# Optimization experiments

Hardware: AMD Instinct MI355X
Metric: run time of the kernel (lower is better)

The kernel has to match this reference:

```python
import jax, jax.numpy as jnp
import numpy as np


def setup_inputs() -> dict:
    key = jax.random.key(0)
    k1, k2 = jax.random.split(key)
    B, P, H, W, D, C = 4, 8, 32, 32, 32, 16
    input_fmap = jax.random.normal(k1, (B, P, H, W, D, C), dtype=jnp.float32)
    # theta ~ identity affine (rows act on [y, x, z, 1]) + small noise so most
    # sampled coordinates fall inside the volume
    base = jnp.concatenate([jnp.eye(3, dtype=jnp.float32), jnp.zeros((3, 1), jnp.float32)], axis=1)
    theta = base[None, None] + 0.1 * jax.random.normal(k2, (B, P, 3, 4), dtype=jnp.float32)
    return {"input_fmap": input_fmap, "theta": theta}


def reference(input_fmap, theta):
    B, P, H, W, D, C = input_fmap.shape
    # --- affine grid generation (matches tf.meshgrid 'xy' indexing) ---
    xs = jnp.arange(W, dtype=jnp.float32)
    ys = jnp.arange(H, dtype=jnp.float32)
    zs = jnp.arange(D, dtype=jnp.float32)
    x_t, y_t, z_t = jnp.meshgrid(xs, ys, zs, indexing="xy")  # each (H, W, D)
    grid = jnp.stack([y_t.ravel(), x_t.ravel(), z_t.ravel(),
                      jnp.ones(H * W * D, jnp.float32)], axis=0)  # (4, HWD)
    batch_grids = jnp.einsum("bpij,jn->bpin", theta, grid)  # (B, P, 3, HWD)
    batch_grids = batch_grids.reshape(B, P, 3, H, W, D)
    y_s = batch_grids[:, :, 0]
    x_s = batch_grids[:, :, 1]
    z_s = batch_grids[:, :, 2]

    # --- trilinear sampling on a 2-voxel zero-padded volume ---
    fmap_p = jnp.pad(input_fmap, ((0, 0), (0, 0), (2, 2), (2, 2), (2, 2), (0, 0)))
    x = x_s + 2.0
    y = y_s + 2.0
    z = z_s + 2.0
    # NOTE: original code clips all three axes with H + 2 (faithful reproduction)
    hi = H + 2
    x0 = jnp.clip(jnp.floor(x).astype(jnp.int32), 0, hi)
    y0 = jnp.clip(jnp.floor(y).astype(jnp.int32), 0, hi)
    z0 = jnp.clip(jnp.floor(z).astype(jnp.int32), 0, hi)
    x1, y1, z1 = x0 + 1, y0 + 1, z0 + 1

    b_idx = jnp.arange(B)[:, None, None, None, None]
    p_idx = jnp.arange(P)[None, :, None, None, None]

    def gather(yy, xx, zz):
        # indices stacked as [y, x, z] in the original -> axes (H_pad, W_pad, D_pad)
        return fmap_p[b_idx, p_idx, yy, xx, zz]  # (B, P, H, W, D, C)

    c000 = gather(y0, x0, z0)
    c001 = gather(y0, x0, z1)
    c010 = gather(y1, x0, z0)
    c011 = gather(y1, x0, z1)
    c100 = gather(y0, x1, z0)
    c101 = gather(y0, x1, z1)
    c110 = gather(y1, x1, z0)
    c111 = gather(y1, x1, z1)

    xd = (x - x0.astype(jnp.float32))[..., None]
    yd = (y - y0.astype(jnp.float32))[..., None]
    zd = (z - z0.astype(jnp.float32))[..., None]

    out = (c000 * (1 - xd) * (1 - yd) * (1 - zd)
           + c100 * xd * (1 - yd) * (1 - zd)
           + c010 * (1 - xd) * yd * (1 - zd)
           + c001 * (1 - xd) * (1 - yd) * zd
           + c101 * xd * (1 - yd) * zd
           + c011 * (1 - xd) * yd * zd
           + c110 * xd * yd * (1 - zd)
           + c111 * xd * yd * zd)
    return out
```

## Files before the change

### kernel.cpp

```cpp
#include <hip/hip_runtime.h>

constexpr int B = 4, P = 8, H = 32, W = 32, D = 32, C = 16;

constexpr int TI = 4, TJ = 4, TK = 8;
constexpr int VOLCAP = 960;

using f32x4 = __attribute__((ext_vector_type(4))) float;
using f16x8 = __attribute__((ext_vector_type(8))) _Float16;

__global__ __launch_bounds__(256) void resample_tile(
    const float* __restrict__ fmap,
    const float* __restrict__ theta,
    float* __restrict__ out)
{
    __shared__ _Float16 sm[VOLCAP * 16];

    const int orig = blockIdx.x;
    const int virt = (orig & 7) * 1024 + (orig >> 3);
    const int bp = virt >> 8;
    const int t6 = virt & 255;
    const int i0 = (t6 >> 5) * TI;
    const int j0 = ((t6 >> 2) & 7) * TJ;
    const int k0 = (t6 & 3) * TK;

    const float4* th4 = (const float4*)(theta + bp * 12);
    const float4 t0 = th4[0];
    const float4 t1 = th4[1];
    const float4 t2 = th4[2];

    const float fi0 = (float)i0, fj0 = (float)j0, fk0 = (float)k0;
    const float pyb = fmaf(t0.x, fi0, fmaf(t0.y, fj0, fmaf(t0.z, fk0, t0.w))) + 2.f;
    const float pxb = fmaf(t1.x, fi0, fmaf(t1.y, fj0, fmaf(t1.z, fk0, t1.w))) + 2.f;
    const float pzb = fmaf(t2.x, fi0, fmaf(t2.y, fj0, fmaf(t2.z, fk0, t2.w))) + 2.f;

    const float eyi = t0.x * (TI - 1), eyj = t0.y * (TJ - 1), eyk = t0.z * (TK - 1);
    const float exi = t1.x * (TI - 1), exj = t1.y * (TJ - 1), exk = t1.z * (TK - 1);
    const float ezi = t2.x * (TI - 1), ezj = t2.y * (TJ - 1), ezk = t2.z * (TK - 1);

    const float pymin = pyb + fminf(eyi, 0.f) + fminf(eyj, 0.f) + fminf(eyk, 0.f);
    const float pymax = pyb + fmaxf(eyi, 0.f) + fmaxf(eyj, 0.f) + fmaxf(eyk, 0.f);
    const float pxmin = pxb + fminf(exi, 0.f) + fminf(exj, 0.f) + fminf(exk, 0.f);
    const float pxmax = pxb + fmaxf(exi, 0.f) + fmaxf(exj, 0.f) + fmaxf(exk, 0.f);
    const float pzmin = pzb + fminf(ezi, 0.f) + fminf(ezj, 0.f) + fminf(ezk, 0.f);
    const float pzmax = pzb + fmaxf(ezi, 0.f) + fmaxf(ezj, 0.f) + fmaxf(ezk, 0.f);

    const int tylo = max(0, min((int)fminf(fmaxf(floorf(pymin), 0.f), 34.f) - 2, 31));
    int       tyhi = min(31, (int)fminf(fmaxf(floorf(pymax), 0.f), 34.f) - 1);
    tyhi = max(tyhi, tylo);
    const int txlo = max(0, min((int)fminf(fmaxf(floorf(pxmin), 0.f), 34.f) - 2, 31));
    int       txhi = min(31, (int)fminf(fmaxf(floorf(pxmax), 0.f), 34.f) - 1);
    txhi = max(txhi, txlo);
    const int tzlo = max(0, min((int)fminf(fmaxf(floorf(pzmin), 0.f), 34.f) - 2, 31));
    int       tzhi = min(31, (int)fminf(fmaxf(floorf(pzmax), 0.f), 34.f) - 1);
    tzhi = max(tzhi, tzlo);

    const int dy = tyhi - tylo + 1;
    const int dx = txhi - txlo + 1;
    const int dz = tzhi - tzlo + 1;
    const int vol = dy * dx * dz;
    const bool fast = (vol <= VOLCAP) && (dy <= 20) && (dx <= 20) && (dz <= 20);

    const float* slice = fmap + bp * (H * W * D * C);

    if (fast) {
        const unsigned mdz = 0xFFFFu / (unsigned)dz + 1u;
        const unsigned mdx = 0xFFFFu / (unsigned)dx + 1u;
        const int nch = vol * 2;
        for (int s = threadIdx.x; s < nch; s += 256) {
            const int vf = s >> 1, hh = s & 1;
            const int row = (int)(((unsigned)vf * mdz) >> 16);
            const int zl  = vf - row * dz;
            const int ry  = (int)(((unsigned)row * mdx) >> 16);
            const int rx  = row - ry * dx;
            const float* g = slice
                + (((tylo + ry) * W + (txlo + rx)) * D + (tzlo + zl)) * C + hh * 8;
            const f32x4 a = *(const f32x4*)g;
            const f32x4 b = *(const f32x4*)(g + 4);
            f16x8 hv;
            hv[0] = (_Float16)a[0]; hv[1] = (_Float16)a[1];
            hv[2] = (_Float16)a[2]; hv[3] = (_Float16)a[3];
            hv[4] = (_Float16)b[0]; hv[5] = (_Float16)b[1];
            hv[6] = (_Float16)b[2]; hv[7] = (_Float16)b[3];
            *(f16x8*)(sm + vf * 16 + hh * 8) = hv;
        }
    }
    __syncthreads();

    const int h8 = threadIdx.x & 1;
    const int v  = threadIdx.x >> 1;
    const int lk = v & 7;
    const int lj = (v >> 3) & 3;
    const int li = v >> 5;

    const float fi = (float)(i0 + li), fj = (float)(j0 + lj), fk = (float)(k0 + lk);
    const float py = fmaf(t0.x, fi, fmaf(t0.y, fj, fmaf(t0.z, fk, t0.w))) + 2.f;
    const float px = fmaf(t1.x, fi, fmaf(t1.y, fj, fmaf(t1.z, fk, t1.w))) + 2.f;
    const float pz = fmaf(t2.x, fi, fmaf(t2.y, fj, fmaf(t2.z, fk, t2.w))) + 2.f;

    const float fy0 = fminf(fmaxf(floorf(py), 0.f), 34.f);
    const float fx0 = fminf(fmaxf(floorf(px), 0.f), 34.f);
    const float fz0 = fminf(fmaxf(floorf(pz), 0.f), 34.f);
    const float yd = py - fy0, xd = px - fx0, zd = pz - fz0;
    const int ty0 = (int)fy0 - 2, tx0 = (int)fx0 - 2, tz0 = (int)fz0 - 2;

    float wy[2], wx[2], wz[2];
    int   iy[2], ix[2], iz[2];
    wy[0] = ((unsigned)ty0       < (unsigned)H) ? (1.0f - yd) : 0.0f;
    wy[1] = ((unsigned)(ty0 + 1) < (unsigned)H) ? yd          : 0.0f;
    wx[0] = ((unsigned)tx0       < (unsigned)W) ? (1.0f - xd) : 0.0f;
    wx[1] = ((unsigned)(tx0 + 1) < (unsigned)W) ? xd          : 0.0f;
    wz[0] = ((unsigned)tz0       < (unsigned)D) ? (1.0f - zd) : 0.0f;
    wz[1] = ((unsigned)(tz0 + 1) < (unsigned)D) ? zd          : 0.0f;
    iy[0] = min(max(ty0, 0), H - 1);  iy[1] = min(max(ty0 + 1, 0), H - 1);
    ix[0] = min(max(tx0, 0), W - 1);  ix[1] = min(max(tx0 + 1, 0), W - 1);
    iz[0] = min(max(tz0, 0), D - 1);  iz[1] = min(max(tz0 + 1, 0), D - 1);

    f32x4 r0, r1;

    if (fast) {
        int ly[2], lx[2], lz[2];
        ly[0] = min(max(iy[0] - tylo, 0), dy - 1);
        ly[1] = min(max(iy[1] - tylo, 0), dy - 1);
        lx[0] = min(max(ix[0] - txlo, 0), dx - 1);
        lx[1] = min(max(ix[1] - txlo, 0), dx - 1);
        lz[0] = min(max(iz[0] - tzlo, 0), dz - 1);
        lz[1] = min(max(iz[1] - tzlo, 0), dz - 1);

        f16x8 aA = 0, aB = 0;
        #pragma unroll
        for (int a = 0; a < 2; ++a)
            #pragma unroll
            for (int b2 = 0; b2 < 2; ++b2)
                #pragma unroll
                for (int c2 = 0; c2 < 2; ++c2) {
                    const int cn = a * 4 + b2 * 2 + c2;
                    const int vf = (ly[a] * dx + lx[b2]) * dz + lz[c2];
                    const f16x8 d = *(const f16x8*)(sm + vf * 16 + h8 * 8);
                    const _Float16 hw = (_Float16)(wy[a] * wx[b2] * wz[c2]);
                    const f16x8 hv = {hw, hw, hw, hw, hw, hw, hw, hw};
                    if (cn < 4) aA += hv * d; else aB += hv * d;
                }
        r0[0] = (float)aA[0] + (float)aB[0];
        r0[1] = (float)aA[1] + (float)aB[1];
        r0[2] = (float)aA[2] + (float)aB[2];
        r0[3] = (float)aA[3] + (float)aB[3];
        r1[0] = (float)aA[4] + (float)aB[4];
        r1[1] = (float)aA[5] + (float)aB[5];
        r1[2] = (float)aA[6] + (float)aB[6];
        r1[3] = (float)aA[7] + (float)aB[7];
    } else {
        const float* gb = slice + h8 * 8;
        f32x4 acc0 = {0,0,0,0}, acc1 = {0,0,0,0};
        #pragma unroll
        for (int a = 0; a < 2; ++a)
            #pragma unroll
            for (int b2 = 0; b2 < 2; ++b2)
                #pragma unroll
                for (int c2 = 0; c2 < 2; ++c2) {
                    const float wgt = wy[a] * wx[b2] * wz[c2];
                    const float* p = gb + ((iy[a] * W + ix[b2]) * D + iz[c2]) * C;
                    acc0 += wgt * *(const f32x4*)p;
                    acc1 += wgt * *(const f32x4*)(p + 4);
                }
        r0 = acc0; r1 = acc1;
    }

    float* op = out + (((bp * H + (i0 + li)) * W + (j0 + lj)) * D + (k0 + lk)) * C
                    + h8 * 8;
    *(f32x4*)op       = r0;
    *(f32x4*)(op + 4) = r1;
}

extern "C" void kernel_launch(void* const* d_in, const int* in_sizes, int n_in,
                              void* d_out, int out_size, void* d_ws, size_t ws_size,
                              hipStream_t stream) {
    const float* fmap  = (const float*)d_in[0];
    const float* theta = (const float*)d_in[1];
    float* out = (float*)d_out;

    const int grid = (B * P * H * W * D) / (TI * TJ * TK);
    resample_tile<<<grid, 256, 0, stream>>>(fmap, theta, out);
}
```

Measured before the change: 28.86 us.

## Double output tile per block and assign one voxel's 16 channels per thread

Doubles the output tile along j (4x8x8 voxels per block), so the neighbourhood staged in shared memory covers more outputs and the grid holds half as many blocks. Each thread now handles all 16 channels of one voxel instead of 8, with full 64-byte loads and stores in both the staging and the compute phase. This is meant to cut redundant halo loads and per-voxel index arithmetic, at the cost of a larger shared-memory buffer, more registers per thread and fewer blocks in flight. The fast path also switches to summing the fp16 partial accumulators in fp16 before converting to fp32.

```diff
diff --git a/kernel.cpp b/kernel.cpp
--- a/kernel.cpp
+++ b/kernel.cpp
@@ -2,8 +2,8 @@
 
 constexpr int B = 4, P = 8, H = 32, W = 32, D = 32, C = 16;
 
-constexpr int TI = 4, TJ = 4, TK = 8;
-constexpr int VOLCAP = 960;
+constexpr int TI = 4, TJ = 8, TK = 8;
+constexpr int VOLCAP = 1152;
 
 using f32x4 = __attribute__((ext_vector_type(4))) float;
 using f16x8 = __attribute__((ext_vector_type(8))) _Float16;
@@ -16,12 +16,12 @@
     __shared__ _Float16 sm[VOLCAP * 16];
 
     const int orig = blockIdx.x;
-    const int virt = (orig & 7) * 1024 + (orig >> 3);
-    const int bp = virt >> 8;
-    const int t6 = virt & 255;
-    const int i0 = (t6 >> 5) * TI;
-    const int j0 = ((t6 >> 2) & 7) * TJ;
-    const int k0 = (t6 & 3) * TK;
+    const int virt = (orig & 7) * 512 + (orig >> 3);
+    const int bp = virt >> 7;
+    const int t7 = virt & 127;
+    const int i0 = (t7 >> 4) * TI;
+    const int j0 = ((t7 >> 2) & 3) * TJ;
+    const int k0 = (t7 & 3) * TK;
 
     const float4* th4 = (const float4*)(theta + bp * 12);
     const float4 t0 = th4[0];
@@ -65,32 +65,36 @@
     if (fast) {
         const unsigned mdz = 0xFFFFu / (unsigned)dz + 1u;
         const unsigned mdx = 0xFFFFu / (unsigned)dx + 1u;
-        const int nch = vol * 2;
-        for (int s = threadIdx.x; s < nch; s += 256) {
-            const int vf = s >> 1, hh = s & 1;
-            const int row = (int)(((unsigned)vf * mdz) >> 16);
-            const int zl  = vf - row * dz;
+        for (int s = threadIdx.x; s < vol; s += 256) {
+            const int row = (int)(((unsigned)s * mdz) >> 16);
+            const int zl  = s - row * dz;
             const int ry  = (int)(((unsigned)row * mdx) >> 16);
             const int rx  = row - ry * dx;
             const float* g = slice
-                + (((tylo + ry) * W + (txlo + rx)) * D + (tzlo + zl)) * C + hh * 8;
-            const f32x4 a = *(const f32x4*)g;
-            const f32x4 b = *(const f32x4*)(g + 4);
-            f16x8 hv;
-            hv[0] = (_Float16)a[0]; hv[1] = (_Float16)a[1];
-            hv[2] = (_Float16)a[2]; hv[3] = (_Float16)a[3];
-            hv[4] = (_Float16)b[0]; hv[5] = (_Float16)b[1];
-            hv[6] = (_Float16)b[2]; hv[7] = (_Float16)b[3];
-            *(f16x8*)(sm + vf * 16 + hh * 8) = hv;
+                + (((tylo + ry) * W + (txlo + rx)) * D + (tzlo + zl)) * C;
+            const f32x4 a  = *(const f32x4*)g;
+            const f32x4 b2 = *(const f32x4*)(g + 4);
+            const f32x4 c  = *(const f32x4*)(g + 8);
+            const f32x4 d4 = *(const f32x4*)(g + 12);
+            f16x8 lo, hi;
+            lo[0] = (_Float16)a[0];  lo[1] = (_Float16)a[1];
+            lo[2] = (_Float16)a[2];  lo[3] = (_Float16)a[3];
+            lo[4] = (_Float16)b2[0]; lo[5] = (_Float16)b2[1];
+            lo[6] = (_Float16)b2[2]; lo[7] = (_Float16)b2[3];
+            hi[0] = (_Float16)c[0];  hi[1] = (_Float16)c[1];
+            hi[2] = (_Float16)c[2];  hi[3] = (_Float16)c[3];
+            hi[4] = (_Float16)d4[0]; hi[5] = (_Float16)d4[1];
+            hi[6] = (_Float16)d4[2]; hi[7] = (_Float16)d4[3];
+            *(f16x8*)(sm + s * 16)     = lo;
+            *(f16x8*)(sm + s * 16 + 8) = hi;
         }
     }
     __syncthreads();
 
-    const int h8 = threadIdx.x & 1;
-    const int v  = threadIdx.x >> 1;
-    const int lk = v & 7;
-    const int lj = (v >> 3) & 3;
-    const int li = v >> 5;
+    const int tid = threadIdx.x;
+    const int lk = tid & 7;
+    const int lj = (tid >> 3) & 7;
+    const int li = tid >> 6;
 
     const float fi = (float)(i0 + li), fj = (float)(j0 + lj), fk = (float)(k0 + lk);
     const float py = fmaf(t0.x, fi, fmaf(t0.y, fj, fmaf(t0.z, fk, t0.w))) + 2.f;
@@ -104,53 +108,59 @@
     const int ty0 = (int)fy0 - 2, tx0 = (int)fx0 - 2, tz0 = (int)fz0 - 2;
 
     float wy[2], wx[2], wz[2];
-    int   iy[2], ix[2], iz[2];
     wy[0] = ((unsigned)ty0       < (unsigned)H) ? (1.0f - yd) : 0.0f;
     wy[1] = ((unsigned)(ty0 + 1) < (unsigned)H) ? yd          : 0.0f;
     wx[0] = ((unsigned)tx0       < (unsigned)W) ? (1.0f - xd) : 0.0f;
     wx[1] = ((unsigned)(tx0 + 1) < (unsigned)W) ? xd          : 0.0f;
     wz[0] = ((unsigned)tz0       < (unsigned)D) ? (1.0f - zd) : 0.0f;
     wz[1] = ((unsigned)(tz0 + 1) < (unsigned)D) ? zd          : 0.0f;
-    iy[0] = min(max(ty0, 0), H - 1);  iy[1] = min(max(ty0 + 1, 0), H - 1);
-    ix[0] = min(max(tx0, 0), W - 1);  ix[1] = min(max(tx0 + 1, 0), W - 1);
-    iz[0] = min(max(tz0, 0), D - 1);  iz[1] = min(max(tz0 + 1, 0), D - 1);
 
-    f32x4 r0, r1;
+    f32x4 r0, r1, r2, r3;
 
     if (fast) {
         int ly[2], lx[2], lz[2];
-        ly[0] = min(max(iy[0] - tylo, 0), dy - 1);
-        ly[1] = min(max(iy[1] - tylo, 0), dy - 1);
-        lx[0] = min(max(ix[0] - txlo, 0), dx - 1);
-        lx[1] = min(max(ix[1] - txlo, 0), dx - 1);
-        lz[0] = min(max(iz[0] - tzlo, 0), dz - 1);
-        lz[1] = min(max(iz[1] - tzlo, 0), dz - 1);
+        ly[0] = min(max(ty0     - tylo, 0), dy - 1);
+        ly[1] = min(max(ty0 + 1 - tylo, 0), dy - 1);
+        lx[0] = min(max(tx0     - txlo, 0), dx - 1);
+        lx[1] = min(max(tx0 + 1 - txlo, 0), dx - 1);
+        lz[0] = min(max(tz0     - tzlo, 0), dz - 1);
+        lz[1] = min(max(tz0 + 1 - tzlo, 0), dz - 1);
 
-        f16x8 aA = 0, aB = 0;
+        f16x8 aA0 = 0, aA1 = 0, aB0 = 0, aB1 = 0;
         #pragma unroll
-        for (int a = 0; a < 2; ++a)
+        for (int a = 0; a < 2; ++a) {
             #pragma unroll
-            for (int b2 = 0; b2 < 2; ++b2)
+            for (int b2 = 0; b2 < 2; ++b2) {
+                const int rowb = (ly[a] * dx + lx[b2]) * dz;
+                const float wyx = wy[a] * wx[b2];
                 #pragma unroll
                 for (int c2 = 0; c2 < 2; ++c2) {
-                    const int cn = a * 4 + b2 * 2 + c2;
-                    const int vf = (ly[a] * dx + lx[b2]) * dz + lz[c2];
-                    const f16x8 d = *(const f16x8*)(sm + vf * 16 + h8 * 8);
-                    const _Float16 hw = (_Float16)(wy[a] * wx[b2] * wz[c2]);
+                    const int vf = rowb + lz[c2];
+                    const f16x8 dlo = *(const f16x8*)(sm + vf * 16);
+                    const f16x8 dhi = *(const f16x8*)(sm + vf * 16 + 8);
+                    const _Float16 hw = (_Float16)(wyx * wz[c2]);
                     const f16x8 hv = {hw, hw, hw, hw, hw, hw, hw, hw};
-                    if (cn < 4) aA += hv * d; else aB += hv * d;
+                    if (a == 0) { aA0 += hv * dlo; aA1 += hv * dhi; }
+                    else        { aB0 += hv * dlo; aB1 += hv * dhi; }
                 }
-        r0[0] = (float)aA[0] + (float)aB[0];
-        r0[1] = (float)aA[1] + (float)aB[1];
-        r0[2] = (float)aA[2] + (float)aB[2];
-        r0[3] = (float)aA[3] + (float)aB[3];
-        r1[0] = (float)aA[4] + (float)aB[4];
-        r1[1] = (float)aA[5] + (float)aB[5];
-        r1[2] = (float)aA[6] + (float)aB[6];
-        r1[3] = (float)aA[7] + (float)aB[7];
+            }
+        }
+        const f16x8 s0 = aA0 + aB0;
+        const f16x8 s1 = aA1 + aB1;
+        r0[0] = (float)s0[0]; r0[1] = (float)s0[1];
+        r0[2] = (float)s0[2]; r0[3] = (float)s0[3];
+        r1[0] = (float)s0[4]; r1[1] = (float)s0[5];
+        r1[2] = (float)s0[6]; r1[3] = (float)s0[7];
+        r2[0] = (float)s1[0]; r2[1] = (float)s1[1];
+        r2[2] = (float)s1[2]; r2[3] = (float)s1[3];
+        r3[0] = (float)s1[4]; r3[1] = (float)s1[5];
+        r3[2] = (float)s1[6]; r3[3] = (float)s1[7];
     } else {
-        const float* gb = slice + h8 * 8;
-        f32x4 acc0 = {0,0,0,0}, acc1 = {0,0,0,0};
+        int iy[2], ix[2], iz[2];
+        iy[0] = min(max(ty0, 0), H - 1);  iy[1] = min(max(ty0 + 1, 0), H - 1);
+        ix[0] = min(max(tx0, 0), W - 1);  ix[1] = min(max(tx0 + 1, 0), W - 1);
+        iz[0] = min(max(tz0, 0), D - 1);  iz[1] = min(max(tz0 + 1, 0), D - 1);
+        f32x4 acc[4] = {{0,0,0,0},{0,0,0,0},{0,0,0,0},{0,0,0,0}};
         #pragma unroll
         for (int a = 0; a < 2; ++a)
             #pragma unroll
@@ -158,17 +168,20 @@
                 #pragma unroll
                 for (int c2 = 0; c2 < 2; ++c2) {
                     const float wgt = wy[a] * wx[b2] * wz[c2];
-                    const float* p = gb + ((iy[a] * W + ix[b2]) * D + iz[c2]) * C;
-                    acc0 += wgt * *(const f32x4*)p;
-                    acc1 += wgt * *(const f32x4*)(p + 4);
+                    const float* p = slice +
+                        ((iy[a] * W + ix[b2]) * D + iz[c2]) * C;
+                    #pragma unroll
+                    for (int q = 0; q < 4; ++q)
+                        acc[q] += wgt * *(const f32x4*)(p + q * 4);
                 }
-        r0 = acc0; r1 = acc1;
+        r0 = acc[0]; r1 = acc[1]; r2 = acc[2]; r3 = acc[3];
     }
 
-    float* op = out + (((bp * H + (i0 + li)) * W + (j0 + lj)) * D + (k0 + lk)) * C
-                    + h8 * 8;
-    *(f32x4*)op       = r0;
-    *(f32x4*)(op + 4) = r1;
+    float* op = out + (((bp * H + (i0 + li)) * W + (j0 + lj)) * D + (k0 + lk)) * C;
+    *(f32x4*)(op)      = r0;
+    *(f32x4*)(op + 4)  = r1;
+    *(f32x4*)(op + 8)  = r2;
+    *(f32x4*)(op + 12) = r3;
 }
 
 extern "C" void kernel_launch(void* const* d_in, const int* in_sizes, int n_in,
```

After: 36.47 us. 1.26x slower.
